# Kernel optimization log

Measured on AMD Instinct MI355X. Metric: run time of the kernel, lower is better.

## Reference

```python
import jax, jax.numpy as jnp
import numpy as np

NUM_EMBEDDINGS = 1024
EMBEDDING_DIM = 256
COMMITMENT_COST = 0.25
DECAY = 0.99
EPS = 1e-05
BATCH = 65536


def setup_inputs() -> dict:
    key = jax.random.key(0)
    k1, k2 = jax.random.split(key, 2)
    z_e = jax.random.normal(k1, (BATCH, EMBEDDING_DIM), dtype=jnp.float32)
    embedding = jax.random.normal(k2, (NUM_EMBEDDINGS, EMBEDDING_DIM), dtype=jnp.float32)
    ema_cluster_size = jnp.zeros((NUM_EMBEDDINGS,), dtype=jnp.float32)
    ema_w = embedding  # buffer initialized as a clone of the codebook
    return {"z_e": z_e, "embedding": embedding,
            "ema_cluster_size": ema_cluster_size, "ema_w": ema_w}


def reference(z_e, embedding, ema_cluster_size, ema_w):
    B, D = z_e.shape
    K = embedding.shape[0]

    # Squared L2 distances: ||z||^2 + ||e||^2 - 2 z.e  -> [B, K]
    z_sq = jnp.sum(z_e * z_e, axis=1, keepdims=True)          # [B, 1]
    e_sq = jnp.sum(embedding * embedding, axis=1)[None, :]    # [1, K]
    ze = jnp.matmul(z_e, embedding.T)                         # [B, K]
    distances = z_sq + e_sq - 2.0 * ze

    encoding_indices = jnp.argmin(distances, axis=1)          # [B]

    # Gather instead of one-hot matmul (same math as encodings @ embedding)
    z_q = embedding[encoding_indices]                         # [B, D]
    z_q_st = z_e + jax.lax.stop_gradient(z_q - z_e)

    vq_loss = COMMITMENT_COST * jnp.mean(
        (jax.lax.stop_gradient(z_q) - z_e) ** 2)

    # EMA statistics (training-mode update); segment_sum == one-hot reductions
    cluster_size = jax.ops.segment_sum(
        jnp.ones((B,), dtype=z_e.dtype), encoding_indices, num_segments=K)
    new_ema_cluster_size = DECAY * ema_cluster_size + (1.0 - DECAY) * cluster_size
    dw = jax.ops.segment_sum(z_e, encoding_indices, num_segments=K)  # [K, D]
    new_ema_w = DECAY * ema_w + (1.0 - DECAY) * dw

    n = jnp.sum(new_ema_cluster_size)
    smoothed = (new_ema_cluster_size + EPS) / (n + K * EPS) * n
    new_embedding = new_ema_w / smoothed[:, None]

    avg_probs = cluster_size / B
    perplexity = jnp.exp(-jnp.sum(avg_probs * jnp.log(avg_probs + 1e-10)))

    return (z_q_st, vq_loss, perplexity, encoding_indices,
            new_embedding, new_ema_cluster_size, new_ema_w)
```

## Files before the change

### kernel.cpp

```cpp
#include <hip/hip_runtime.h>
#include <hip/hip_bf16.h>
#include <math.h>

#define BATCH 65536
#define DIM 256
#define KC 1024
#define COMMIT 0.25f
#define DECAY 0.99f
#define EPSV 1e-5f

#define O_ZQ   0
#define O_LOSS 16777216
#define O_PERP 16777217
#define O_IDX  16777218
#define O_EMB  16842754
#define O_NCS  17104898
#define O_NEW  17105922

typedef __attribute__((ext_vector_type(8))) short bf16x8;
typedef __attribute__((ext_vector_type(4))) float f32x4;

__device__ __forceinline__ unsigned short bf16_rne(float x) {
    unsigned u = __builtin_bit_cast(unsigned, x);
    unsigned r = (u + 0x7FFFu + ((u >> 16) & 1u)) >> 16;
    return (unsigned short)r;
}
__device__ __forceinline__ float bf16_to_f(unsigned short h) {
    unsigned u = ((unsigned)h) << 16;
    return __builtin_bit_cast(float, u);
}

__global__ __launch_bounds__(256) void zero_kernel(float* __restrict__ dw,
                                                   int* __restrict__ counts,
                                                   float* __restrict__ loss_part) {
    int i = blockIdx.x * 256 + threadIdx.x;
    if (i < KC * DIM) dw[i] = 0.0f;
    if (i < KC) counts[i] = 0;
    if (i < 256) loss_part[i] = 0.0f;
}

__global__ __launch_bounds__(64) void prep_kernel(const float* __restrict__ emb,
                                                  unsigned short* __restrict__ ehi,
                                                  unsigned short* __restrict__ elo,
                                                  float* __restrict__ e_sq) {
    int k = blockIdx.x;
    int lane = threadIdx.x;
    const float4* ep = (const float4*)(emb + (size_t)k * DIM);
    float4 e = ep[lane];
    float x[4] = {e.x, e.y, e.z, e.w};
    unsigned h[4], l[4];
    float s = 0.0f;
    #pragma unroll
    for (int j = 0; j < 4; ++j) {
        h[j] = bf16_rne(x[j]);
        l[j] = bf16_rne(x[j] - bf16_to_f((unsigned short)h[j]));
        s += x[j] * x[j];
    }
    uint2 ph = make_uint2(h[0] | (h[1] << 16), h[2] | (h[3] << 16));
    uint2 pl = make_uint2(l[0] | (l[1] << 16), l[2] | (l[3] << 16));
    ((uint2*)(ehi + (size_t)k * DIM))[lane] = ph;
    ((uint2*)(elo + (size_t)k * DIM))[lane] = pl;
    for (int off = 32; off; off >>= 1) s += __shfl_down(s, off, 64);
    if (lane == 0) e_sq[k] = s;
}

#define CH_ROWS 64
#define ROW_US 264
__global__ __launch_bounds__(256, 2) void argmin_kernel(
        const float* __restrict__ z_e,
        const unsigned short* __restrict__ ehi,
        const unsigned short* __restrict__ elo,
        const float* __restrict__ e_sq,
        int* __restrict__ idx_out, float* __restrict__ idx_f_out) {
    __shared__ __align__(16) unsigned short bhi_s[CH_ROWS * ROW_US];
    __shared__ __align__(16) unsigned short blo_s[CH_ROWS * ROW_US];
    __shared__ float esq_s[KC];

    int tid = threadIdx.x;
    int w = tid >> 6;
    int lane = tid & 63;
    int m16 = lane & 15;
    int quad = lane >> 4;
    int base_m = blockIdx.x * 128 + w * 32;

    #pragma unroll
    for (int i = 0; i < 4; ++i) esq_s[tid + i * 256] = e_sq[tid + i * 256];

    bf16x8 ahi[2][8], alo[2][8];
    #pragma unroll
    for (int f = 0; f < 2; ++f) {
        const float* zr = z_e + (size_t)(base_m + f * 16 + m16) * DIM;
        #pragma unroll
        for (int ks = 0; ks < 8; ++ks) {
            const float4* p = (const float4*)(zr + ks * 32 + quad * 8);
            float4 x0 = p[0], x1 = p[1];
            float xs[8] = {x0.x, x0.y, x0.z, x0.w, x1.x, x1.y, x1.z, x1.w};
            #pragma unroll
            for (int j = 0; j < 8; ++j) {
                unsigned short h = bf16_rne(xs[j]);
                unsigned short l = bf16_rne(xs[j] - bf16_to_f(h));
                ahi[f][ks][j] = (short)h;
                alo[f][ks][j] = (short)l;
            }
        }
    }

    float best0[4] = {1e30f, 1e30f, 1e30f, 1e30f};
    float best1[4] = {1e30f, 1e30f, 1e30f, 1e30f};
    int bk0[4] = {0, 0, 0, 0};
    int bk1[4] = {0, 0, 0, 0};

    for (int chunk = 0; chunk < 16; ++chunk) {
        __syncthreads();
        const int4* gh = (const int4*)(ehi + (size_t)chunk * CH_ROWS * DIM);
        const int4* gl = (const int4*)(elo + (size_t)chunk * CH_ROWS * DIM);
        #pragma unroll
        for (int i = 0; i < 8; ++i) {
            int c = tid + i * 256;
            int r = c >> 5;
            int col = c & 31;
            int4 vh = gh[c];
            int4 vl = gl[c];
            *(int4*)((char*)bhi_s + r * 528 + col * 16) = vh;
            *(int4*)((char*)blo_s + r * 528 + col * 16) = vl;
        }
        __syncthreads();

        #pragma unroll
        for (int f = 0; f < 4; ++f) {
            f32x4 acc0 = {0.f, 0.f, 0.f, 0.f};
            f32x4 acc1 = {0.f, 0.f, 0.f, 0.f};
            const unsigned short* bh_base = bhi_s + (f * 16 + m16) * ROW_US + quad * 8;
            const unsigned short* bl_base = blo_s + (f * 16 + m16) * ROW_US + quad * 8;
            #pragma unroll
            for (int ks = 0; ks < 8; ++ks) {
                bf16x8 bh = *(const bf16x8*)(bh_base + ks * 32);
                bf16x8 bl = *(const bf16x8*)(bl_base + ks * 32);
                acc0 = __builtin_amdgcn_mfma_f32_16x16x32_bf16(ahi[0][ks], bh, acc0, 0, 0, 0);
                acc1 = __builtin_amdgcn_mfma_f32_16x16x32_bf16(ahi[1][ks], bh, acc1, 0, 0, 0);
                acc0 = __builtin_amdgcn_mfma_f32_16x16x32_bf16(ahi[0][ks], bl, acc0, 0, 0, 0);
                acc1 = __builtin_amdgcn_mfma_f32_16x16x32_bf16(ahi[1][ks], bl, acc1, 0, 0, 0);
                acc0 = __builtin_amdgcn_mfma_f32_16x16x32_bf16(alo[0][ks], bh, acc0, 0, 0, 0);
                acc1 = __builtin_amdgcn_mfma_f32_16x16x32_bf16(alo[1][ks], bh, acc1, 0, 0, 0);
            }
            int col = chunk * 64 + f * 16 + m16;
            float es = esq_s[col];
            #pragma unroll
            for (int r = 0; r < 4; ++r) {
                float d0 = es - 2.0f * acc0[r];
                float d1 = es - 2.0f * acc1[r];
                if (d0 < best0[r]) { best0[r] = d0; bk0[r] = col; }
                if (d1 < best1[r]) { best1[r] = d1; bk1[r] = col; }
            }
        }
    }

    #pragma unroll
    for (int off = 1; off < 16; off <<= 1) {
        #pragma unroll
        for (int r = 0; r < 4; ++r) {
            float ov0 = __shfl_xor(best0[r], off, 64);
            int   ok0 = __shfl_xor(bk0[r], off, 64);
            if (ov0 < best0[r] || (ov0 == best0[r] && ok0 < bk0[r])) { best0[r] = ov0; bk0[r] = ok0; }
            float ov1 = __shfl_xor(best1[r], off, 64);
            int   ok1 = __shfl_xor(bk1[r], off, 64);
            if (ov1 < best1[r] || (ov1 == best1[r] && ok1 < bk1[r])) { best1[r] = ov1; bk1[r] = ok1; }
        }
    }
    if (m16 == 0) {
        #pragma unroll
        for (int r = 0; r < 4; ++r) {
            int row0 = base_m + quad * 4 + r;
            int row1 = base_m + 16 + quad * 4 + r;
            idx_out[row0] = bk0[r];
            idx_f_out[row0] = (float)bk0[r];
            idx_out[row1] = bk1[r];
            idx_f_out[row1] = (float)bk1[r];
        }
    }
}

__global__ __launch_bounds__(256) void hist_kernel(const int* __restrict__ idx,
                                                   int* __restrict__ counts) {
    __shared__ int h[KC];
    int t = threadIdx.x;
    #pragma unroll
    for (int i = t; i < KC; i += 256) h[i] = 0;
    __syncthreads();
    int base = blockIdx.x * (BATCH / 128);
    #pragma unroll
    for (int i = t; i < BATCH / 128; i += 256) atomicAdd(&h[idx[base + i]], 1);
    __syncthreads();
    #pragma unroll
    for (int i = t; i < KC; i += 256) if (h[i]) atomicAdd(&counts[i], h[i]);
}

__global__ __launch_bounds__(1024) void prefix_kernel(const int* __restrict__ counts,
                                                      int* __restrict__ cursor) {
    __shared__ int sc[KC];
    int t = threadIdx.x;
    int c = counts[t];
    sc[t] = c;
    __syncthreads();
    for (int off = 1; off < KC; off <<= 1) {
        int v = 0;
        if (t >= off) v = sc[t - off];
        __syncthreads();
        if (t >= off) sc[t] += v;
        __syncthreads();
    }
    cursor[t] = sc[t] - c;
}

__global__ __launch_bounds__(256) void scatter_rows_kernel(
        const int* __restrict__ idx, int* __restrict__ cursor,
        int* __restrict__ sorted_rows) {
    int i = blockIdx.x * 256 + threadIdx.x;
    int k = idx[i];
    int pos = atomicAdd(&cursor[k], 1);
    sorted_rows[pos] = i;
}

#define SEG 64
__global__ __launch_bounds__(256) void dw_zq_kernel(
        const float* __restrict__ z_e, const float* __restrict__ emb,
        const int* __restrict__ idx, const int* __restrict__ sorted_rows,
        float* __restrict__ zq_out, float* __restrict__ dw,
        float* __restrict__ loss_part) {
    __shared__ int rows_s[SEG];
    __shared__ int keys_s[SEG];
    int t = threadIdx.x;
    int base = blockIdx.x * SEG;
    if (t < SEG) {
        int r = sorted_rows[base + t];
        rows_s[t] = r;
        keys_s[t] = idx[r];
    }
    __syncthreads();

    float acc = 0.0f;
    float lsum = 0.0f;
    int kprev = keys_s[0];
    for (int i = 0; i < SEG; ++i) {
        int row = rows_s[i];
        int k = keys_s[i];
        float z = z_e[(size_t)row * DIM + t];
        float q = emb[(size_t)k * DIM + t];
        zq_out[(size_t)row * DIM + t] = z + (q - z);
        float d = q - z;
        lsum += d * d;
        if (k != kprev) {
            atomicAdd(&dw[(size_t)kprev * DIM + t], acc);
            acc = 0.0f;
            kprev = k;
        }
        acc += z;
    }
    atomicAdd(&dw[(size_t)kprev * DIM + t], acc);

    __shared__ float red[256];
    red[t] = lsum;
    __syncthreads();
    for (int s = 128; s; s >>= 1) {
        if (t < s) red[t] += red[t + s];
        __syncthreads();
    }
    if (t == 0) atomicAdd(&loss_part[blockIdx.x & 255], red[0]);
}

__global__ __launch_bounds__(1024) void finalize_cluster(
        const float* __restrict__ ema_cs, const int* __restrict__ counts,
        const float* __restrict__ loss_part, float* __restrict__ out,
        float* __restrict__ n_ws) {
    __shared__ float s1[1024];
    __shared__ float s2[1024];
    __shared__ float s3[1024];
    int t = threadIdx.x;
    float c = (float)counts[t];
    float ncs = DECAY * ema_cs[t] + (1.0f - DECAY) * c;
    out[O_NCS + t] = ncs;
    float p = c / (float)BATCH;
    s1[t] = ncs;
    s2[t] = p * logf(p + 1e-10f);
    s3[t] = (t < 256) ? loss_part[t] : 0.0f;
    __syncthreads();
    for (int s = 512; s; s >>= 1) {
        if (t < s) { s1[t] += s1[t + s]; s2[t] += s2[t + s]; s3[t] += s3[t + s]; }
        __syncthreads();
    }
    if (t == 0) {
        n_ws[0] = s1[0];
        out[O_PERP] = expf(-s2[0]);
        out[O_LOSS] = COMMIT * s3[0] / (float)((size_t)BATCH * DIM);
    }
}

__global__ __launch_bounds__(256) void finalize_emb(
        const float* __restrict__ ema_w, const float* __restrict__ dw,
        const float* __restrict__ ncs_arr, const float* __restrict__ n_ws,
        float* __restrict__ out_emb, float* __restrict__ out_emaw) {
    int k = blockIdx.x;
    int d = threadIdx.x;
    size_t i = (size_t)k * DIM + d;
    float w = DECAY * ema_w[i] + (1.0f - DECAY) * dw[i];
    out_emaw[i] = w;
    float n = n_ws[0];
    float ncs = ncs_arr[k];
    float smoothed = (ncs + EPSV) / (n + (float)KC * EPSV) * n;
    out_emb[i] = w / smoothed;
}

extern "C" void kernel_launch(void* const* d_in, const int* in_sizes, int n_in,
                              void* d_out, int out_size, void* d_ws, size_t ws_size,
                              hipStream_t stream) {
    const float* z_e    = (const float*)d_in[0];
    const float* emb    = (const float*)d_in[1];
    const float* ema_cs = (const float*)d_in[2];
    const float* ema_w  = (const float*)d_in[3];
    float* out = (float*)d_out;
    float* ws = (float*)d_ws;

    float* dw            = ws;
    unsigned short* ehi  = (unsigned short*)(dw + KC * DIM);
    unsigned short* elo  = ehi + KC * DIM;
    float* e_sq          = (float*)(elo + KC * DIM);
    int* idx             = (int*)(e_sq + KC);
    int* counts          = idx + BATCH;
    int* cursor          = counts + KC;
    int* sorted_rows     = cursor + KC;
    float* loss_part     = (float*)(sorted_rows + BATCH);
    float* n_ws          = loss_part + 256;

    zero_kernel<<<dim3(1024), dim3(256), 0, stream>>>(dw, counts, loss_part);
    prep_kernel<<<dim3(KC), dim3(64), 0, stream>>>(emb, ehi, elo, e_sq);
    argmin_kernel<<<dim3(BATCH / 128), dim3(256), 0, stream>>>(
        z_e, ehi, elo, e_sq, idx, out + O_IDX);
    hist_kernel<<<dim3(128), dim3(256), 0, stream>>>(idx, counts);
    prefix_kernel<<<dim3(1), dim3(1024), 0, stream>>>(counts, cursor);
    scatter_rows_kernel<<<dim3(BATCH / 256), dim3(256), 0, stream>>>(
        idx, cursor, sorted_rows);
    dw_zq_kernel<<<dim3(BATCH / SEG), dim3(256), 0, stream>>>(
        z_e, emb, idx, sorted_rows, out + O_ZQ, dw, loss_part);
    finalize_cluster<<<dim3(1), dim3(1024), 0, stream>>>(
        ema_cs, counts, loss_part, out, n_ws);
    finalize_emb<<<dim3(KC), dim3(256), 0, stream>>>(
        ema_w, dw, out + O_NCS, n_ws, out + O_EMB, out + O_NEW);
}
```

Measured before the change: 283.7 us.

## Double-buffer codebook chunks in LDS with register prefetch in argmin kernel

Splits the codebook staging into 32-row chunks held in two LDS buffers. The next chunk is loaded into registers before the MFMA work on the current chunk and written to the other buffer afterwards, so only one barrier is needed per chunk. This is meant to hide global-load latency behind compute and remove the serialized load-then-compute pattern. In exchange it uses more registers for the prefetch and runs twice as many, smaller iterations with a barrier each.

```diff
diff --git a/kernel.cpp b/kernel.cpp
--- a/kernel.cpp
+++ b/kernel.cpp
@@ -64,7 +64,7 @@
     if (lane == 0) e_sq[k] = s;
 }
 
-#define CH_ROWS 64
+#define CH 32
 #define ROW_US 264
 __global__ __launch_bounds__(256, 2) void argmin_kernel(
         const float* __restrict__ z_e,
@@ -72,8 +72,8 @@
         const unsigned short* __restrict__ elo,
         const float* __restrict__ e_sq,
         int* __restrict__ idx_out, float* __restrict__ idx_f_out) {
-    __shared__ __align__(16) unsigned short bhi_s[CH_ROWS * ROW_US];
-    __shared__ __align__(16) unsigned short blo_s[CH_ROWS * ROW_US];
+    __shared__ __align__(16) unsigned short bhi_s[2][CH * ROW_US];
+    __shared__ __align__(16) unsigned short blo_s[2][CH * ROW_US];
     __shared__ float esq_s[KC];
 
     int tid = threadIdx.x;
@@ -105,33 +105,42 @@
         }
     }
 
+    const int4* gh = (const int4*)ehi;
+    const int4* gl = (const int4*)elo;
+    int4 ph[4], pl[4];
+    #pragma unroll
+    for (int i = 0; i < 4; ++i) { ph[i] = gh[tid + i * 256]; pl[i] = gl[tid + i * 256]; }
+    #pragma unroll
+    for (int i = 0; i < 4; ++i) {
+        int c16 = tid + i * 256;
+        int r = c16 >> 5, col = c16 & 31;
+        *(int4*)((char*)&bhi_s[0][0] + r * 528 + col * 16) = ph[i];
+        *(int4*)((char*)&blo_s[0][0] + r * 528 + col * 16) = pl[i];
+    }
+    __syncthreads();
+
     float best0[4] = {1e30f, 1e30f, 1e30f, 1e30f};
     float best1[4] = {1e30f, 1e30f, 1e30f, 1e30f};
     int bk0[4] = {0, 0, 0, 0};
     int bk1[4] = {0, 0, 0, 0};
 
-    for (int chunk = 0; chunk < 16; ++chunk) {
-        __syncthreads();
-        const int4* gh = (const int4*)(ehi + (size_t)chunk * CH_ROWS * DIM);
-        const int4* gl = (const int4*)(elo + (size_t)chunk * CH_ROWS * DIM);
+    for (int c = 0; c < 32; ++c) {
+        int buf = c & 1;
+        if (c < 31) {
+            int b16 = (c + 1) * 1024;
+            #pragma unroll
+            for (int i = 0; i < 4; ++i) {
+                ph[i] = gh[b16 + tid + i * 256];
+                pl[i] = gl[b16 + tid + i * 256];
+            }
+        }
+
         #pragma unroll
-        for (int i = 0; i < 8; ++i) {
-            int c = tid + i * 256;
-            int r = c >> 5;
-            int col = c & 31;
-            int4 vh = gh[c];
-            int4 vl = gl[c];
-            *(int4*)((char*)bhi_s + r * 528 + col * 16) = vh;
-            *(int4*)((char*)blo_s + r * 528 + col * 16) = vl;
-        }
-        __syncthreads();
-
-        #pragma unroll
-        for (int f = 0; f < 4; ++f) {
+        for (int f = 0; f < 2; ++f) {
             f32x4 acc0 = {0.f, 0.f, 0.f, 0.f};
             f32x4 acc1 = {0.f, 0.f, 0.f, 0.f};
-            const unsigned short* bh_base = bhi_s + (f * 16 + m16) * ROW_US + quad * 8;
-            const unsigned short* bl_base = blo_s + (f * 16 + m16) * ROW_US + quad * 8;
+            const unsigned short* bh_base = &bhi_s[buf][(f * 16 + m16) * ROW_US + quad * 8];
+            const unsigned short* bl_base = &blo_s[buf][(f * 16 + m16) * ROW_US + quad * 8];
             #pragma unroll
             for (int ks = 0; ks < 8; ++ks) {
                 bf16x8 bh = *(const bf16x8*)(bh_base + ks * 32);
@@ -143,7 +152,7 @@
                 acc0 = __builtin_amdgcn_mfma_f32_16x16x32_bf16(alo[0][ks], bh, acc0, 0, 0, 0);
                 acc1 = __builtin_amdgcn_mfma_f32_16x16x32_bf16(alo[1][ks], bh, acc1, 0, 0, 0);
             }
-            int col = chunk * 64 + f * 16 + m16;
+            int col = c * 32 + f * 16 + m16;
             float es = esq_s[col];
             #pragma unroll
             for (int r = 0; r < 4; ++r) {
@@ -152,6 +161,17 @@
                 if (d0 < best0[r]) { best0[r] = d0; bk0[r] = col; }
                 if (d1 < best1[r]) { best1[r] = d1; bk1[r] = col; }
             }
+        }
+
+        if (c < 31) {
+            #pragma unroll
+            for (int i = 0; i < 4; ++i) {
+                int c16 = tid + i * 256;
+                int r = c16 >> 5, col = c16 & 31;
+                *(int4*)((char*)&bhi_s[buf ^ 1][0] + r * 528 + col * 16) = ph[i];
+                *(int4*)((char*)&blo_s[buf ^ 1][0] + r * 528 + col * 16) = pl[i];
+            }
+            __syncthreads();
         }
     }
 
```

Measured after the change: 285.8 us. About the same (+0.7%).
